# Optimization experiments

Measured on AMD Instinct MI355X. Metric: run time of the kernel, lower is better.

Reference implementation:

```python
import jax, jax.numpy as jnp
import numpy as np

EPS = 1e-5

def gn(x, w, b):
    # torch GroupNorm(num_groups=1, C) on [N, C]: normalize over channels per row
    m = jnp.mean(x, axis=-1, keepdims=True)
    v = jnp.mean((x - m) ** 2, axis=-1, keepdims=True)
    return (x - m) * jax.lax.rsqrt(v + EPS) * w + b

def att_layer(agts, ctr_d, hi, wi, nodes, p):
    (Wd1, bd1, Wd2, gnd2_w, gnd2_b, Wq, gnq_w, gnq_b,
     Wc1, gnc1_w, gnc1_b, Wc2, Wa, gnn_w, gnn_b, Wl, gnl_w, gnl_b) = p
    res = agts
    # dist MLP on edge ctr differences [E,2]
    d = jax.nn.relu(ctr_d @ Wd1.T + bd1)                     # [E, n_ctx]
    d = jax.nn.relu(gn(d @ Wd2.T, gnd2_w, gnd2_b))           # [E, n_ctx]
    # query from gathered actor features
    q = jax.nn.relu(gn(agts[hi] @ Wq.T, gnq_w, gnq_b))       # [E, n_ctx]
    # context: concat(dist, query, gathered lane feats) -> MLP
    cf = jnp.concatenate([d, q, nodes[wi]], axis=-1)         # [E, 3*n_ctx]
    cf = jax.nn.relu(gn(cf @ Wc1.T, gnc1_w, gnc1_b))         # [E, n_agt]
    cf = cf @ Wc2.T                                          # [E, n_agt]
    # scatter-aggregate onto actors
    a = agts @ Wa.T
    a = a.at[hi].add(cf)
    a = jax.nn.relu(gn(a, gnn_w, gnn_b))
    a = gn(a @ Wl.T, gnl_w, gnl_b)  # Linear with act=False
    return jax.nn.relu(a + res)

def setup_inputs() -> dict:
    key = jax.random.key(0)
    ks = jax.random.split(key, 20)
    M, N, E, D = 4000, 20000, 150000, 128
    s2 = 1.0 / np.sqrt(2.0)
    s128 = 1.0 / np.sqrt(128.0)
    s384 = 1.0 / np.sqrt(384.0)
    inp = {}
    inp["actors"] = jax.random.normal(ks[0], (M, D), jnp.float32)
    inp["nodes"] = jax.random.normal(ks[1], (N, D), jnp.float32)
    inp["actor_ctrs"] = jax.random.uniform(ks[2], (M, 2), jnp.float32)
    inp["node_ctrs"] = jax.random.uniform(ks[3], (N, 2), jnp.float32)
    inp["hi"] = jax.random.randint(ks[4], (E,), 0, M, dtype=jnp.int32)
    inp["wi"] = jax.random.randint(ks[5], (E,), 0, N, dtype=jnp.int32)
    inp["Wd1"] = jax.random.normal(ks[6], (2, D, 2), jnp.float32) * s2
    inp["bd1"] = jnp.zeros((2, D), jnp.float32)
    inp["Wd2"] = jax.random.normal(ks[7], (2, D, D), jnp.float32) * s128
    inp["gnd2_w"] = jnp.ones((2, D), jnp.float32)
    inp["gnd2_b"] = jnp.zeros((2, D), jnp.float32)
    inp["Wq"] = jax.random.normal(ks[8], (2, D, D), jnp.float32) * s128
    inp["gnq_w"] = jnp.ones((2, D), jnp.float32)
    inp["gnq_b"] = jnp.zeros((2, D), jnp.float32)
    inp["Wc1"] = jax.random.normal(ks[9], (2, D, 3 * D), jnp.float32) * s384
    inp["gnc1_w"] = jnp.ones((2, D), jnp.float32)
    inp["gnc1_b"] = jnp.zeros((2, D), jnp.float32)
    inp["Wc2"] = jax.random.normal(ks[10], (2, D, D), jnp.float32) * s128
    inp["Wa"] = jax.random.normal(ks[11], (2, D, D), jnp.float32) * s128
    inp["gnn_w"] = jnp.ones((2, D), jnp.float32)
    inp["gnn_b"] = jnp.zeros((2, D), jnp.float32)
    inp["Wl"] = jax.random.normal(ks[12], (2, D, D), jnp.float32) * s128
    inp["gnl_w"] = jnp.ones((2, D), jnp.float32)
    inp["gnl_b"] = jnp.zeros((2, D), jnp.float32)
    return inp

def reference(actors, nodes, actor_ctrs, node_ctrs, hi, wi,
              Wd1, bd1, Wd2, gnd2_w, gnd2_b, Wq, gnq_w, gnq_b,
              Wc1, gnc1_w, gnc1_b, Wc2, Wa, gnn_w, gnn_b, Wl, gnl_w, gnl_b):
    ctr_d = actor_ctrs[hi] - node_ctrs[wi]  # [E, 2], same edges for both layers
    stacked = (Wd1, bd1, Wd2, gnd2_w, gnd2_b, Wq, gnq_w, gnq_b,
               Wc1, gnc1_w, gnc1_b, Wc2, Wa, gnn_w, gnn_b, Wl, gnl_w, gnl_b)
    agts = actors
    for i in range(2):  # two Att layers
        p = tuple(t[i] for t in stacked)
        agts = att_layer(agts, ctr_d, hi, wi, nodes, p)
    return agts
```

## Files before the change

### kernel.cpp

```cpp
#include <hip/hip_runtime.h>

#define M_ACT 4000
#define NNODE 20000
#define NE 150000
#define DD 128
#define NT_E 586
#define NB_N2 313
#define ASTR 136
#define WSTR 72
#define BSTR 136

typedef __attribute__((ext_vector_type(8))) short bh8;
typedef __attribute__((ext_vector_type(4))) float vf4;

#define MFMA16(a, b, c) __builtin_amdgcn_mfma_f32_16x16x32_bf16((a), (b), (c), 0, 0, 0)
#define LGKM0() __asm__ volatile("s_waitcnt lgkmcnt(0)" ::: "memory")

__device__ __forceinline__ unsigned short f2bf(float f) {
    unsigned u = __float_as_uint(f);
    u = (u + 0x7fffu + ((u >> 16) & 1u)) >> 16;
    return (unsigned short)u;
}
__device__ __forceinline__ float bf2f(unsigned short s) {
    return __uint_as_float(((unsigned)s) << 16);
}

__device__ __forceinline__ void gn_stats8(const vf4* acc, float* mean, float* rs) {
    float s[4], q[4];
#pragma unroll
    for (int i = 0; i < 4; i++) {
        float a = 0.f, b = 0.f;
#pragma unroll
        for (int t = 0; t < 8; t++) { float v = acc[t][i]; a += v; b += v * v; }
        s[i] = a; q[i] = b;
    }
#pragma unroll
    for (int m = 1; m < 16; m <<= 1) {
#pragma unroll
        for (int i = 0; i < 4; i++) {
            s[i] += __shfl_xor(s[i], m, 64);
            q[i] += __shfl_xor(q[i], m, 64);
        }
    }
#pragma unroll
    for (int i = 0; i < 4; i++) {
        float mu = s[i] * (1.0f / 128.0f);
        float var = q[i] * (1.0f / 128.0f) - mu * mu;
        mean[i] = mu;
        rs[i] = rsqrtf(var + 1e-5f);
    }
}

template <bool RELU>
__device__ __forceinline__ void gn_to_lds(const vf4* acc, const float* __restrict__ gw,
                                          const float* __restrict__ gb, unsigned short* sm,
                                          int stride, int cb, int r0, int grp, int lm) {
    float mean[4], rs[4];
    gn_stats8(acc, mean, rs);
#pragma unroll
    for (int t = 0; t < 8; t++) {
        int c = 16 * t + lm;
        float w = gw[c], b = gb[c];
#pragma unroll
        for (int i = 0; i < 4; i++) {
            float y = (acc[t][i] - mean[i]) * rs[i] * w + b;
            if (RELU) y = fmaxf(y, 0.0f);
            sm[(r0 + grp * 4 + i) * stride + cb + c] = f2bf(y);
        }
    }
}

__device__ __forceinline__ void load_chunk(const unsigned short* __restrict__ src,
                                           unsigned short* dst, int tid) {
    for (int idx = tid; idx < 1152; idx += 256) {
        *(uint4*)&dst[idx * 8] = *(const uint4*)&src[idx * 8];
    }
}

__global__ __launch_bounds__(256, 2) void q2_kernel(const float* __restrict__ agts,
                                                    const unsigned short* __restrict__ wblob_l,
                                                    const float* __restrict__ gnq_w,
                                                    const float* __restrict__ gnq_b,
                                                    float* __restrict__ Q2) {
    __shared__ unsigned short smA[64 * ASTR];
    __shared__ unsigned short smW[128 * WSTR];
    const int tid = threadIdx.x;
    const int wave = tid >> 6, lane = tid & 63, grp = lane >> 4, lm = lane & 15;
    const int m0 = blockIdx.x * 64;
    const int r0 = wave * 16;
    const int arow = r0 + lm;

    for (int idx = tid; idx < 64 * 32; idx += 256) {
        int r = idx >> 5, q = idx & 31;
        int m = m0 + r;
        if (m >= M_ACT) m = 0;
        const float4 v = *(const float4*)(agts + (size_t)m * DD + q * 4);
        unsigned lo = (unsigned)f2bf(v.x) | ((unsigned)f2bf(v.y) << 16);
        unsigned hi2 = (unsigned)f2bf(v.z) | ((unsigned)f2bf(v.w) << 16);
        *(uint2*)&smA[r * ASTR + q * 4] = make_uint2(lo, hi2);
    }
    __syncthreads();

    vf4 acc[8];
#pragma unroll
    for (int t = 0; t < 8; t++) acc[t] = (vf4){0.f, 0.f, 0.f, 0.f};
    for (int ch = 0; ch < 2; ch++) {
        load_chunk(wblob_l + (2 + ch) * 9216, smW, tid);
        __syncthreads();
#pragma unroll
        for (int k0 = 0; k0 < 64; k0 += 32) {
            bh8 a = *(const bh8*)&smA[arow * ASTR + ch * 64 + k0 + grp * 8];
#pragma unroll
            for (int t = 0; t < 8; t++) {
                bh8 b = *(const bh8*)&smW[(16 * t + lm) * WSTR + k0 + grp * 8];
                acc[t] = MFMA16(a, b, acc[t]);
            }
        }
        __syncthreads();
    }
    gn_to_lds<true>(acc, gnq_w, gnq_b, smA, ASTR, 0, r0, grp, lm);

#pragma unroll
    for (int t = 0; t < 8; t++) acc[t] = (vf4){0.f, 0.f, 0.f, 0.f};
    for (int ch = 0; ch < 2; ch++) {
        load_chunk(wblob_l + (6 + ch) * 9216, smW, tid);
        __syncthreads();
#pragma unroll
        for (int k0 = 0; k0 < 64; k0 += 32) {
            bh8 a = *(const bh8*)&smA[arow * ASTR + ch * 64 + k0 + grp * 8];
#pragma unroll
            for (int t = 0; t < 8; t++) {
                bh8 b = *(const bh8*)&smW[(16 * t + lm) * WSTR + k0 + grp * 8];
                acc[t] = MFMA16(a, b, acc[t]);
            }
        }
        __syncthreads();
    }
#pragma unroll
    for (int t = 0; t < 8; t++) {
        int c = 16 * t + lm;
#pragma unroll
        for (int i = 0; i < 4; i++) {
            int m = m0 + r0 + grp * 4 + i;
            if (m < M_ACT) Q2[(size_t)m * DD + c] = acc[t][i];
        }
    }
}

__global__ __launch_bounds__(256, 2) void n2_kernel(const float* __restrict__ nodes,
                                                    const unsigned short* __restrict__ wblob,
                                                    float* __restrict__ N2_0,
                                                    float* __restrict__ N2_1) {
    __shared__ unsigned short smA[64 * ASTR];
    __shared__ unsigned short smW[128 * WSTR];
    const int half = blockIdx.x / NB_N2;
    const int bx = blockIdx.x - half * NB_N2;
    const unsigned short* wblob_l = wblob + (size_t)half * 16 * 9216;
    float* __restrict__ N2 = half ? N2_1 : N2_0;
    const int tid = threadIdx.x;
    const int wave = tid >> 6, lane = tid & 63, grp = lane >> 4, lm = lane & 15;
    const int n0 = bx * 64;
    const int r0 = wave * 16;
    const int arow = r0 + lm;

    for (int idx = tid; idx < 64 * 32; idx += 256) {
        int r = idx >> 5, q = idx & 31;
        int n = n0 + r;
        if (n >= NNODE) n = 0;
        const float4 v = *(const float4*)(nodes + (size_t)n * DD + q * 4);
        unsigned lo = (unsigned)f2bf(v.x) | ((unsigned)f2bf(v.y) << 16);
        unsigned hi2 = (unsigned)f2bf(v.z) | ((unsigned)f2bf(v.w) << 16);
        *(uint2*)&smA[r * ASTR + q * 4] = make_uint2(lo, hi2);
    }
    __syncthreads();

    vf4 acc[8];
#pragma unroll
    for (int t = 0; t < 8; t++) acc[t] = (vf4){0.f, 0.f, 0.f, 0.f};
    for (int ch = 0; ch < 2; ch++) {
        load_chunk(wblob_l + (8 + ch) * 9216, smW, tid);
        __syncthreads();
#pragma unroll
        for (int k0 = 0; k0 < 64; k0 += 32) {
            bh8 a = *(const bh8*)&smA[arow * ASTR + ch * 64 + k0 + grp * 8];
#pragma unroll
            for (int t = 0; t < 8; t++) {
                bh8 b = *(const bh8*)&smW[(16 * t + lm) * WSTR + k0 + grp * 8];
                acc[t] = MFMA16(a, b, acc[t]);
            }
        }
        __syncthreads();
    }
#pragma unroll
    for (int t = 0; t < 8; t++) {
        int c = 16 * t + lm;
#pragma unroll
        for (int i = 0; i < 4; i++) {
            int n = n0 + r0 + grp * 4 + i;
            if (n < NNODE) N2[(size_t)n * DD + c] = acc[t][i];
        }
    }
}

__global__ __launch_bounds__(512, 2) void edge_kernel(
    const float* __restrict__ actor_ctrs, const float* __restrict__ node_ctrs,
    const float* __restrict__ Wd1_l, const float* __restrict__ bd1_l,
    const float* __restrict__ Q2, const float* __restrict__ N2,
    const int* __restrict__ hi_s, const int* __restrict__ wi_s,
    const unsigned short* __restrict__ wblob_l,
    const float* __restrict__ gnd2_w, const float* __restrict__ gnd2_b,
    const float* __restrict__ gnc1_w, const float* __restrict__ gnc1_b,
    float* __restrict__ ssum, int* __restrict__ ctr) {
    __shared__ unsigned short smW[4 * 9216];
    __shared__ unsigned short smBuf[8][32 * BSTR];
    __shared__ float smWd1[3][128];
    __shared__ int smTile;
    {
        const int src0[4] = {0, 1, 4, 5};
#pragma unroll
        for (int s = 0; s < 4; s++)
            for (int idx = threadIdx.x; idx < 1152; idx += 512)
                *(uint4*)&smW[s * 9216 + idx * 8] =
                    *(const uint4*)&wblob_l[src0[s] * 9216 + idx * 8];
        for (int t = threadIdx.x; t < 128; t += 512) {
            smWd1[0][t] = Wd1_l[2 * t + 0];
            smWd1[1][t] = Wd1_l[2 * t + 1];
            smWd1[2][t] = bd1_l[t];
        }
    }
    const int wave = threadIdx.x >> 6, lane = threadIdx.x & 63;
    const int grp = lane >> 4, lm = lane & 15;
    unsigned short* buf = smBuf[wave];

    while (true) {
        __syncthreads();
        if (threadIdx.x == 0) smTile = atomicAdd(ctr, 1);
        __syncthreads();
        int tile = smTile;
        if (tile >= NT_E) break;
        int j0 = tile * 256 + wave * 32;
        if (j0 >= NE) continue;

        vf4 acc[2][8];
        int hg[2][4], wg[2][4];
        float cx[2], cy[2];
#pragma unroll
        for (int rt = 0; rt < 2; rt++) {
            int r = j0 + rt * 16 + lm;
            if (r > NE - 1) r = NE - 1;
            int hr = hi_s[r], wr = wi_s[r];
            cx[rt] = actor_ctrs[hr * 2 + 0] - node_ctrs[wr * 2 + 0];
            cy[rt] = actor_ctrs[hr * 2 + 1] - node_ctrs[wr * 2 + 1];
#pragma unroll
            for (int i = 0; i < 4; i++) {
                int j = j0 + rt * 16 + grp * 4 + i;
                if (j > NE - 1) j = NE - 1;
                hg[rt][i] = hi_s[j];
                wg[rt][i] = wi_s[j];
            }
        }
        bh8 a1[2][4];
#pragma unroll
        for (int ks = 0; ks < 4; ks++) {
            float wx[8], wy[8], wb[8];
#pragma unroll
            for (int e = 0; e < 8; e++) {
                int c = ks * 32 + grp * 8 + e;
                wx[e] = smWd1[0][c];
                wy[e] = smWd1[1][c];
                wb[e] = smWd1[2][c];
            }
#pragma unroll
            for (int rt = 0; rt < 2; rt++) {
                bh8 v;
#pragma unroll
                for (int e = 0; e < 8; e++) {
                    float x = fmaf(cy[rt], wy[e], fmaf(cx[rt], wx[e], wb[e]));
                    v[e] = (short)f2bf(fmaxf(x, 0.f));
                }
                a1[rt][ks] = v;
            }
        }
#pragma unroll
        for (int rt = 0; rt < 2; rt++)
#pragma unroll
            for (int t = 0; t < 8; t++) acc[rt][t] = (vf4){0.f, 0.f, 0.f, 0.f};
#pragma unroll
        for (int ks = 0; ks < 4; ks++) {
            bh8 B[8];
#pragma unroll
            for (int t = 0; t < 8; t++)
                B[t] = *(const bh8*)&smW[(ks >> 1) * 9216 + (16 * t + lm) * WSTR +
                                         (ks & 1) * 32 + grp * 8];
#pragma unroll
            for (int rt = 0; rt < 2; rt++)
#pragma unroll
                for (int t = 0; t < 8; t++) acc[rt][t] = MFMA16(a1[rt][ks], B[t], acc[rt][t]);
        }
        LGKM0();
#pragma unroll
        for (int rt = 0; rt < 2; rt++) {
            float mean[4], rs[4];
            gn_stats8(acc[rt], mean, rs);
#pragma unroll
            for (int t = 0; t < 8; t++) {
                int c = 16 * t + lm;
                float w = gnd2_w[c], b = gnd2_b[c];
#pragma unroll
                for (int i = 0; i < 4; i++) {
                    float y = (acc[rt][t][i] - mean[i]) * rs[i] * w + b;
                    buf[(rt * 16 + grp * 4 + i) * BSTR + c] = f2bf(fmaxf(y, 0.f));
                }
            }
        }
        LGKM0();
#pragma unroll
        for (int rt = 0; rt < 2; rt++)
#pragma unroll
            for (int t = 0; t < 8; t++) acc[rt][t] = (vf4){0.f, 0.f, 0.f, 0.f};
#pragma unroll
        for (int ks = 0; ks < 4; ks++) {
            bh8 B[8];
#pragma unroll
            for (int t = 0; t < 8; t++)
                B[t] = *(const bh8*)&smW[(2 + (ks >> 1)) * 9216 + (16 * t + lm) * WSTR +
                                         (ks & 1) * 32 + grp * 8];
#pragma unroll
            for (int rt = 0; rt < 2; rt++) {
                bh8 a = *(const bh8*)&buf[(rt * 16 + lm) * BSTR + ks * 32 + grp * 8];
#pragma unroll
                for (int t = 0; t < 8; t++) acc[rt][t] = MFMA16(a, B[t], acc[rt][t]);
            }
        }
#pragma unroll
        for (int rt = 0; rt < 2; rt++)
#pragma unroll
            for (int t = 0; t < 8; t++) {
                int c = 16 * t + lm;
#pragma unroll
                for (int i = 0; i < 4; i++)
                    acc[rt][t][i] +=
                        Q2[(size_t)hg[rt][i] * DD + c] + N2[(size_t)wg[rt][i] * DD + c];
            }
#pragma unroll
        for (int rt = 0; rt < 2; rt++) {
            float mean[4], rs[4];
            gn_stats8(acc[rt], mean, rs);
#pragma unroll
            for (int t = 0; t < 8; t++) {
                int c = 16 * t + lm;
                float w = gnc1_w[c], b = gnc1_b[c];
#pragma unroll
                for (int i = 0; i < 4; i++) {
                    float y = (acc[rt][t][i] - mean[i]) * rs[i] * w + b;
                    acc[rt][t][i] = fmaxf(y, 0.f);
                }
            }
        }
        {
            int hrem[2][4];
#pragma unroll
            for (int rt = 0; rt < 2; rt++)
#pragma unroll
                for (int i = 0; i < 4; i++) {
                    int j = j0 + rt * 16 + grp * 4 + i;
                    hrem[rt][i] = (j < NE) ? hg[rt][i] : -1;
                }
            while (true) {
                int hmin = 0x7fffffff;
#pragma unroll
                for (int rt = 0; rt < 2; rt++)
#pragma unroll
                    for (int i = 0; i < 4; i++)
                        if (hrem[rt][i] >= 0 && hrem[rt][i] < hmin) hmin = hrem[rt][i];
                hmin = min(hmin, __shfl_xor(hmin, 16, 64));
                hmin = min(hmin, __shfl_xor(hmin, 32, 64));
                if (hmin == 0x7fffffff) break;
                float p[8];
#pragma unroll
                for (int t = 0; t < 8; t++) p[t] = 0.f;
#pragma unroll
                for (int rt = 0; rt < 2; rt++)
#pragma unroll
                    for (int i = 0; i < 4; i++)
                        if (hrem[rt][i] == hmin) {
#pragma unroll
                            for (int t = 0; t < 8; t++) p[t] += acc[rt][t][i];
                            hrem[rt][i] = -1;
                        }
#pragma unroll
                for (int t = 0; t < 8; t++) {
                    p[t] += __shfl_xor(p[t], 16, 64);
                    p[t] += __shfl_xor(p[t], 32, 64);
                }
                if (grp == 0) {
#pragma unroll
                    for (int t = 0; t < 8; t++)
                        atomicAdd(&ssum[(size_t)hmin * DD + 16 * t + lm], p[t]);
                }
            }
        }
    }
}

__global__ __launch_bounds__(256, 2) void actor_kernel(
    const float* __restrict__ agts, const float* __restrict__ ssum,
    const float* __restrict__ gnn_w, const float* __restrict__ gnn_b,
    const float* __restrict__ gnl_w, const float* __restrict__ gnl_b,
    const unsigned short* __restrict__ wblob_l, float* __restrict__ dst) {
    __shared__ unsigned short smA[64 * ASTR];
    __shared__ unsigned short smW[128 * WSTR];
    const int tid = threadIdx.x;
    const int wave = tid >> 6, lane = tid & 63, grp = lane >> 4, lm = lane & 15;
    const int m0 = blockIdx.x * 64;
    const int r0 = wave * 16;
    const int arow = r0 + lm;

    for (int idx = tid; idx < 64 * 32; idx += 256) {
        int r = idx >> 5, q = idx & 31;
        int m = m0 + r;
        if (m >= M_ACT) m = 0;
        const float4 v = *(const float4*)(ssum + (size_t)m * DD + q * 4);
        unsigned lo = (unsigned)f2bf(v.x) | ((unsigned)f2bf(v.y) << 16);
        unsigned hi2 = (unsigned)f2bf(v.z) | ((unsigned)f2bf(v.w) << 16);
        *(uint2*)&smA[r * ASTR + q * 4] = make_uint2(lo, hi2);
    }
    __syncthreads();

    vf4 acc[8];
#pragma unroll
    for (int t = 0; t < 8; t++) acc[t] = (vf4){0.f, 0.f, 0.f, 0.f};
    for (int ch = 0; ch < 2; ch++) {
        load_chunk(wblob_l + (10 + ch) * 9216, smW, tid);
        __syncthreads();
#pragma unroll
        for (int k0 = 0; k0 < 64; k0 += 32) {
            bh8 a = *(const bh8*)&smA[arow * ASTR + ch * 64 + k0 + grp * 8];
#pragma unroll
            for (int t = 0; t < 8; t++) {
                bh8 b = *(const bh8*)&smW[(16 * t + lm) * WSTR + k0 + grp * 8];
                acc[t] = MFMA16(a, b, acc[t]);
            }
        }
        __syncthreads();
    }
    for (int idx = tid; idx < 64 * 32; idx += 256) {
        int r = idx >> 5, q = idx & 31;
        int m = m0 + r;
        if (m >= M_ACT) m = 0;
        const float4 v = *(const float4*)(agts + (size_t)m * DD + q * 4);
        unsigned lo = (unsigned)f2bf(v.x) | ((unsigned)f2bf(v.y) << 16);
        unsigned hi2 = (unsigned)f2bf(v.z) | ((unsigned)f2bf(v.w) << 16);
        *(uint2*)&smA[r * ASTR + q * 4] = make_uint2(lo, hi2);
    }
    __syncthreads();
    for (int ch = 0; ch < 2; ch++) {
        load_chunk(wblob_l + (12 + ch) * 9216, smW, tid);
        __syncthreads();
#pragma unroll
        for (int k0 = 0; k0 < 64; k0 += 32) {
            bh8 a = *(const bh8*)&smA[arow * ASTR + ch * 64 + k0 + grp * 8];
#pragma unroll
            for (int t = 0; t < 8; t++) {
                bh8 b = *(const bh8*)&smW[(16 * t + lm) * WSTR + k0 + grp * 8];
                acc[t] = MFMA16(a, b, acc[t]);
            }
        }
        __syncthreads();
    }
    gn_to_lds<true>(acc, gnn_w, gnn_b, smA, ASTR, 0, r0, grp, lm);

#pragma unroll
    for (int t = 0; t < 8; t++) acc[t] = (vf4){0.f, 0.f, 0.f, 0.f};
    for (int ch = 0; ch < 2; ch++) {
        load_chunk(wblob_l + (14 + ch) * 9216, smW, tid);
        __syncthreads();
#pragma unroll
        for (int k0 = 0; k0 < 64; k0 += 32) {
            bh8 a = *(const bh8*)&smA[arow * ASTR + ch * 64 + k0 + grp * 8];
#pragma unroll
            for (int t = 0; t < 8; t++) {
                bh8 b = *(const bh8*)&smW[(16 * t + lm) * WSTR + k0 + grp * 8];
                acc[t] = MFMA16(a, b, acc[t]);
            }
        }
        __syncthreads();
    }
    {
        float mean[4], rs[4];
        gn_stats8(acc, mean, rs);
#pragma unroll
        for (int t = 0; t < 8; t++) {
            int c = 16 * t + lm;
            float w = gnl_w[c], b = gnl_b[c];
#pragma unroll
            for (int i = 0; i < 4; i++) {
                int m = m0 + r0 + grp * 4 + i;
                if (m < M_ACT) {
                    float y = (acc[t][i] - mean[i]) * rs[i] * w + b;
                    y += agts[(size_t)m * DD + c];
                    dst[(size_t)m * DD + c] = fmaxf(y, 0.f);
                }
            }
        }
    }
}

__global__ void hist_kernel(const int* __restrict__ hi, int* __restrict__ hist) {
    int e = blockIdx.x * 256 + threadIdx.x;
    if (e < NE) atomicAdd(&hist[hi[e]], 1);
}

__global__ void scan_kernel(const int* __restrict__ hist, int* __restrict__ offs,
                            int* __restrict__ cursor) {
    __shared__ int part[256];
    int t = threadIdx.x;
    int base = t * 16;
    int s = 0;
    if (base < M_ACT)
        for (int i = 0; i < 16; i++) s += hist[base + i];
    part[t] = s;
    __syncthreads();
    for (int d = 1; d < 256; d <<= 1) {
        int u = (t >= d) ? part[t - d] : 0;
        __syncthreads();
        part[t] += u;
        __syncthreads();
    }
    int excl = part[t] - s;
    if (base < M_ACT) {
        int run = excl;
        for (int i = 0; i < 16; i++) {
            offs[base + i] = run;
            cursor[base + i] = run;
            run += hist[base + i];
        }
        if (base + 16 == M_ACT) offs[M_ACT] = run;
    }
}

__global__ void scatter_kernel(const int* __restrict__ hi, const int* __restrict__ wi,
                               int* __restrict__ cursor, int* __restrict__ hi_s,
                               int* __restrict__ wi_s) {
    int e = blockIdx.x * 256 + threadIdx.x;
    if (e < NE) {
        int h = hi[e];
        int p = atomicAdd(&cursor[h], 1);
        hi_s[p] = h;
        wi_s[p] = wi[e];
    }
}

__global__ void convert_kernel(const float* __restrict__ Wd2, const float* __restrict__ Wq,
                               const float* __restrict__ Wc1, const float* __restrict__ Wc2,
                               const float* __restrict__ Wa, const float* __restrict__ Wl,
                               unsigned short* __restrict__ wblob) {
    int ci = blockIdx.x;
    int l = ci >> 4, r = ci & 15;
    const float* src;
    int kc, K;
    if (r < 2)       { src = Wd2 + l * 16384; kc = r;      K = 128; }
    else if (r < 4)  { src = Wq  + l * 16384; kc = r - 2;  K = 128; }
    else if (r < 10) { src = Wc1 + l * 49152; kc = r - 4;  K = 384; }
    else if (r < 12) { src = Wc2 + l * 16384; kc = r - 10; K = 128; }
    else if (r < 14) { src = Wa  + l * 16384; kc = r - 12; K = 128; }
    else             { src = Wl  + l * 16384; kc = r - 14; K = 128; }
    unsigned short* dst = wblob + (size_t)ci * 9216;
    for (int idx = threadIdx.x; idx < 9216; idx += 256) {
        int n = idx / 72, kk = idx - n * 72;
        float v = (kk < 64) ? src[n * K + kc * 64 + kk] : 0.f;
        dst[idx] = f2bf(v);
    }
}

extern "C" void kernel_launch(void* const* d_in, const int* in_sizes, int n_in,
                              void* d_out, int out_size, void* d_ws, size_t ws_size,
                              hipStream_t stream) {
    const float* actors = (const float*)d_in[0];
    const float* nodes = (const float*)d_in[1];
    const float* actor_ctrs = (const float*)d_in[2];
    const float* node_ctrs = (const float*)d_in[3];
    const int* hi = (const int*)d_in[4];
    const int* wi = (const int*)d_in[5];
    const float* Wd1 = (const float*)d_in[6];
    const float* bd1 = (const float*)d_in[7];
    const float* Wd2 = (const float*)d_in[8];
    const float* gnd2_w = (const float*)d_in[9];
    const float* gnd2_b = (const float*)d_in[10];
    const float* Wq = (const float*)d_in[11];
    const float* gnq_w = (const float*)d_in[12];
    const float* gnq_b = (const float*)d_in[13];
    const float* Wc1 = (const float*)d_in[14];
    const float* gnc1_w = (const float*)d_in[15];
    const float* gnc1_b = (const float*)d_in[16];
    const float* Wc2 = (const float*)d_in[17];
    const float* Wa = (const float*)d_in[18];
    const float* gnn_w = (const float*)d_in[19];
    const float* gnn_b = (const float*)d_in[20];
    const float* Wl = (const float*)d_in[21];
    const float* gnl_w = (const float*)d_in[22];
    const float* gnl_b = (const float*)d_in[23];
    float* out = (float*)d_out;

    char* ws = (char*)d_ws;
    unsigned short* wblob = (unsigned short*)ws;  ws += 2 * 16 * 9216 * 2;
    float* Q2 = (float*)ws;                       ws += (size_t)M_ACT * DD * 4;
    float* N2_0 = (float*)ws;                     ws += (size_t)NNODE * DD * 4;
    float* N2_1 = (float*)ws;                     ws += (size_t)NNODE * DD * 4;
    float* ssum0 = (float*)ws;                    ws += (size_t)M_ACT * DD * 4;
    float* ssum1 = (float*)ws;                    ws += (size_t)M_ACT * DD * 4;
    float* A1 = (float*)ws;                       ws += (size_t)M_ACT * DD * 4;
    int* hist = (int*)ws;                         ws += M_ACT * 4;
    int* offs = (int*)ws;                         ws += (M_ACT + 4) * 4;
    int* cursor = (int*)ws;                       ws += M_ACT * 4;
    int* hi_s = (int*)ws;                         ws += NE * 4;
    int* wi_s = (int*)ws;                         ws += NE * 4;
    int* ctr4 = (int*)ws;                         ws += 16;

    hipMemsetAsync(hist, 0, M_ACT * 4, stream);
    hipMemsetAsync(ctr4, 0, 16, stream);
    hipMemsetAsync(ssum0, 0, (size_t)M_ACT * DD * 4 * 2, stream);
    hist_kernel<<<(NE + 255) / 256, 256, 0, stream>>>(hi, hist);
    scan_kernel<<<1, 256, 0, stream>>>(hist, offs, cursor);
    scatter_kernel<<<(NE + 255) / 256, 256, 0, stream>>>(hi, wi, cursor, hi_s, wi_s);
    convert_kernel<<<32, 256, 0, stream>>>(Wd2, Wq, Wc1, Wc2, Wa, Wl, wblob);

    const unsigned short* wb0 = wblob;
    const unsigned short* wb1 = wblob + 16 * 9216;
    const int AB = (M_ACT + 63) / 64;

    n2_kernel<<<2 * NB_N2, 256, 0, stream>>>(nodes, wblob, N2_0, N2_1);

    q2_kernel<<<AB, 256, 0, stream>>>(actors, wb0, gnq_w, gnq_b, Q2);
    edge_kernel<<<256, 512, 0, stream>>>(actor_ctrs, node_ctrs, Wd1, bd1, Q2, N2_0, hi_s,
                                         wi_s, wb0, gnd2_w, gnd2_b, gnc1_w, gnc1_b, ssum0,
                                         &ctr4[0]);
    actor_kernel<<<AB, 256, 0, stream>>>(actors, ssum0, gnn_w, gnn_b, gnl_w, gnl_b, wb0, A1);
    q2_kernel<<<AB, 256, 0, stream>>>(A1, wb1, gnq_w + 128, gnq_b + 128, Q2);
    edge_kernel<<<256, 512, 0, stream>>>(actor_ctrs, node_ctrs, Wd1 + 256, bd1 + 128, Q2,
                                         N2_1, hi_s, wi_s, wb1, gnd2_w + 128, gnd2_b + 128,
                                         gnc1_w + 128, gnc1_b + 128, ssum1, &ctr4[1]);
    actor_kernel<<<AB, 256, 0, stream>>>(A1, ssum1, gnn_w + 128, gnn_b + 128, gnl_w + 128,
                                         gnl_b + 128, wb1, out);
}
```

Measured before the change: 320.9 us.

## Merge setup, scatter, projection and actor kernels to cut launch count

The three memsets become one. The histogram and weight conversion run as one setup launch. The edge scatter, node projections and first-layer query projection run as one heterogeneous launch. The layer-0 actor update is fused with the layer-1 query projection so A1 is reused from LDS. This removes several kernel launches and serialization gaps plus a global round trip for A1. The cost is heterogeneous blocks whose work may be unbalanced, and more code per kernel.

```diff
diff --git a/kernel.cpp b/kernel.cpp
--- a/kernel.cpp
+++ b/kernel.cpp
@@ -6,6 +6,8 @@
 #define DD 128
 #define NT_E 586
 #define NB_N2 313
+#define HB 587
+#define AB 63
 #define ASTR 136
 #define WSTR 72
 #define BSTR 136
@@ -77,19 +79,186 @@
     }
 }
 
-__global__ __launch_bounds__(256, 2) void q2_kernel(const float* __restrict__ agts,
-                                                    const unsigned short* __restrict__ wblob_l,
-                                                    const float* __restrict__ gnq_w,
-                                                    const float* __restrict__ gnq_b,
-                                                    float* __restrict__ Q2) {
+__device__ __forceinline__ void q2_body(unsigned short* smA, unsigned short* smW,
+                                        const unsigned short* __restrict__ wq,
+                                        const unsigned short* __restrict__ wc,
+                                        const float* __restrict__ gnq_w,
+                                        const float* __restrict__ gnq_b,
+                                        float* __restrict__ Q2, int m0, int tid) {
+    const int wave = tid >> 6, lane = tid & 63, grp = lane >> 4, lm = lane & 15;
+    const int r0 = wave * 16;
+    const int arow = r0 + lm;
+    vf4 acc[8];
+#pragma unroll
+    for (int t = 0; t < 8; t++) acc[t] = (vf4){0.f, 0.f, 0.f, 0.f};
+    for (int ch = 0; ch < 2; ch++) {
+        load_chunk(wq + ch * 9216, smW, tid);
+        __syncthreads();
+#pragma unroll
+        for (int k0 = 0; k0 < 64; k0 += 32) {
+            bh8 a = *(const bh8*)&smA[arow * ASTR + ch * 64 + k0 + grp * 8];
+#pragma unroll
+            for (int t = 0; t < 8; t++) {
+                bh8 b = *(const bh8*)&smW[(16 * t + lm) * WSTR + k0 + grp * 8];
+                acc[t] = MFMA16(a, b, acc[t]);
+            }
+        }
+        __syncthreads();
+    }
+    gn_to_lds<true>(acc, gnq_w, gnq_b, smA, ASTR, 0, r0, grp, lm);
+
+#pragma unroll
+    for (int t = 0; t < 8; t++) acc[t] = (vf4){0.f, 0.f, 0.f, 0.f};
+    for (int ch = 0; ch < 2; ch++) {
+        load_chunk(wc + ch * 9216, smW, tid);
+        __syncthreads();
+#pragma unroll
+        for (int k0 = 0; k0 < 64; k0 += 32) {
+            bh8 a = *(const bh8*)&smA[arow * ASTR + ch * 64 + k0 + grp * 8];
+#pragma unroll
+            for (int t = 0; t < 8; t++) {
+                bh8 b = *(const bh8*)&smW[(16 * t + lm) * WSTR + k0 + grp * 8];
+                acc[t] = MFMA16(a, b, acc[t]);
+            }
+        }
+        __syncthreads();
+    }
+#pragma unroll
+    for (int t = 0; t < 8; t++) {
+        int c = 16 * t + lm;
+#pragma unroll
+        for (int i = 0; i < 4; i++) {
+            int m = m0 + r0 + grp * 4 + i;
+            if (m < M_ACT) Q2[(size_t)m * DD + c] = acc[t][i];
+        }
+    }
+}
+
+__global__ void setup_kernel(const int* __restrict__ hi, int* __restrict__ hist,
+                             const float* __restrict__ Wd2, const float* __restrict__ Wq,
+                             const float* __restrict__ Wc1, const float* __restrict__ Wc2,
+                             const float* __restrict__ Wa, const float* __restrict__ Wl,
+                             unsigned short* __restrict__ wblob) {
+    int b = blockIdx.x;
+    if (b < HB) {
+        int e = b * 256 + threadIdx.x;
+        if (e < NE) atomicAdd(&hist[hi[e]], 1);
+        return;
+    }
+    int ci = b - HB;
+    int l = ci >> 4, r = ci & 15;
+    const float* src;
+    int kc, K;
+    if (r < 2)       { src = Wd2 + l * 16384; kc = r;      K = 128; }
+    else if (r < 4)  { src = Wq  + l * 16384; kc = r - 2;  K = 128; }
+    else if (r < 10) { src = Wc1 + l * 49152; kc = r - 4;  K = 384; }
+    else if (r < 12) { src = Wc2 + l * 16384; kc = r - 10; K = 128; }
+    else if (r < 14) { src = Wa  + l * 16384; kc = r - 12; K = 128; }
+    else             { src = Wl  + l * 16384; kc = r - 14; K = 128; }
+    unsigned short* dst = wblob + (size_t)ci * 9216;
+    for (int idx = threadIdx.x; idx < 9216; idx += 256) {
+        int n = idx / 72, kk = idx - n * 72;
+        float v = (kk < 64) ? src[n * K + kc * 64 + kk] : 0.f;
+        dst[idx] = f2bf(v);
+    }
+}
+
+__global__ void scan_kernel(const int* __restrict__ hist, int* __restrict__ cursor) {
+    __shared__ int part[256];
+    int t = threadIdx.x;
+    int base = t * 16;
+    int s = 0;
+    if (base < M_ACT)
+        for (int i = 0; i < 16; i++) s += hist[base + i];
+    part[t] = s;
+    __syncthreads();
+    for (int d = 1; d < 256; d <<= 1) {
+        int u = (t >= d) ? part[t - d] : 0;
+        __syncthreads();
+        part[t] += u;
+        __syncthreads();
+    }
+    int excl = part[t] - s;
+    if (base < M_ACT) {
+        int run = excl;
+        for (int i = 0; i < 16; i++) {
+            cursor[base + i] = run;
+            run += hist[base + i];
+        }
+    }
+}
+
+__global__ __launch_bounds__(256, 2) void mega0_kernel(
+    const int* __restrict__ hi, const int* __restrict__ wi, int* __restrict__ cursor,
+    int* __restrict__ hi_s, int* __restrict__ wi_s, const float* __restrict__ nodes,
+    const unsigned short* __restrict__ wblob, float* __restrict__ N2_0,
+    float* __restrict__ N2_1, const float* __restrict__ agts,
+    const float* __restrict__ gnq_w, const float* __restrict__ gnq_b,
+    float* __restrict__ Q2) {
     __shared__ unsigned short smA[64 * ASTR];
     __shared__ unsigned short smW[128 * WSTR];
     const int tid = threadIdx.x;
+    int b = blockIdx.x;
+    if (b < HB) {
+        int e = b * 256 + tid;
+        if (e < NE) {
+            int h = hi[e];
+            int p = atomicAdd(&cursor[h], 1);
+            hi_s[p] = h;
+            wi_s[p] = wi[e];
+        }
+        return;
+    }
+    b -= HB;
     const int wave = tid >> 6, lane = tid & 63, grp = lane >> 4, lm = lane & 15;
-    const int m0 = blockIdx.x * 64;
     const int r0 = wave * 16;
     const int arow = r0 + lm;
-
+    if (b < 2 * NB_N2) {
+        const int half = b / NB_N2;
+        const int bx = b - half * NB_N2;
+        const unsigned short* wblob_l = wblob + (size_t)half * 16 * 9216;
+        float* __restrict__ N2 = half ? N2_1 : N2_0;
+        const int n0 = bx * 64;
+        for (int idx = tid; idx < 64 * 32; idx += 256) {
+            int r = idx >> 5, q = idx & 31;
+            int n = n0 + r;
+            if (n >= NNODE) n = 0;
+            const float4 v = *(const float4*)(nodes + (size_t)n * DD + q * 4);
+            unsigned lo = (unsigned)f2bf(v.x) | ((unsigned)f2bf(v.y) << 16);
+            unsigned hi2 = (unsigned)f2bf(v.z) | ((unsigned)f2bf(v.w) << 16);
+            *(uint2*)&smA[r * ASTR + q * 4] = make_uint2(lo, hi2);
+        }
+        __syncthreads();
+        vf4 acc[8];
+#pragma unroll
+        for (int t = 0; t < 8; t++) acc[t] = (vf4){0.f, 0.f, 0.f, 0.f};
+        for (int ch = 0; ch < 2; ch++) {
+            load_chunk(wblob_l + (8 + ch) * 9216, smW, tid);
+            __syncthreads();
+#pragma unroll
+            for (int k0 = 0; k0 < 64; k0 += 32) {
+                bh8 a = *(const bh8*)&smA[arow * ASTR + ch * 64 + k0 + grp * 8];
+#pragma unroll
+                for (int t = 0; t < 8; t++) {
+                    bh8 bb = *(const bh8*)&smW[(16 * t + lm) * WSTR + k0 + grp * 8];
+                    acc[t] = MFMA16(a, bb, acc[t]);
+                }
+            }
+            __syncthreads();
+        }
+#pragma unroll
+        for (int t = 0; t < 8; t++) {
+            int c = 16 * t + lm;
+#pragma unroll
+            for (int i = 0; i < 4; i++) {
+                int n = n0 + r0 + grp * 4 + i;
+                if (n < NNODE) N2[(size_t)n * DD + c] = acc[t][i];
+            }
+        }
+        return;
+    }
+    b -= 2 * NB_N2;
+    const int m0 = b * 64;
     for (int idx = tid; idx < 64 * 32; idx += 256) {
         int r = idx >> 5, q = idx & 31;
         int m = m0 + r;
@@ -100,106 +269,7 @@
         *(uint2*)&smA[r * ASTR + q * 4] = make_uint2(lo, hi2);
     }
     __syncthreads();
-
-    vf4 acc[8];
-#pragma unroll
-    for (int t = 0; t < 8; t++) acc[t] = (vf4){0.f, 0.f, 0.f, 0.f};
-    for (int ch = 0; ch < 2; ch++) {
-        load_chunk(wblob_l + (2 + ch) * 9216, smW, tid);
-        __syncthreads();
-#pragma unroll
-        for (int k0 = 0; k0 < 64; k0 += 32) {
-            bh8 a = *(const bh8*)&smA[arow * ASTR + ch * 64 + k0 + grp * 8];
-#pragma unroll
-            for (int t = 0; t < 8; t++) {
-                bh8 b = *(const bh8*)&smW[(16 * t + lm) * WSTR + k0 + grp * 8];
-                acc[t] = MFMA16(a, b, acc[t]);
-            }
-        }
-        __syncthreads();
-    }
-    gn_to_lds<true>(acc, gnq_w, gnq_b, smA, ASTR, 0, r0, grp, lm);
-
-#pragma unroll
-    for (int t = 0; t < 8; t++) acc[t] = (vf4){0.f, 0.f, 0.f, 0.f};
-    for (int ch = 0; ch < 2; ch++) {
-        load_chunk(wblob_l + (6 + ch) * 9216, smW, tid);
-        __syncthreads();
-#pragma unroll
-        for (int k0 = 0; k0 < 64; k0 += 32) {
-            bh8 a = *(const bh8*)&smA[arow * ASTR + ch * 64 + k0 + grp * 8];
-#pragma unroll
-            for (int t = 0; t < 8; t++) {
-                bh8 b = *(const bh8*)&smW[(16 * t + lm) * WSTR + k0 + grp * 8];
-                acc[t] = MFMA16(a, b, acc[t]);
-            }
-        }
-        __syncthreads();
-    }
-#pragma unroll
-    for (int t = 0; t < 8; t++) {
-        int c = 16 * t + lm;
-#pragma unroll
-        for (int i = 0; i < 4; i++) {
-            int m = m0 + r0 + grp * 4 + i;
-            if (m < M_ACT) Q2[(size_t)m * DD + c] = acc[t][i];
-        }
-    }
-}
-
-__global__ __launch_bounds__(256, 2) void n2_kernel(const float* __restrict__ nodes,
-                                                    const unsigned short* __restrict__ wblob,
-                                                    float* __restrict__ N2_0,
-                                                    float* __restrict__ N2_1) {
-    __shared__ unsigned short smA[64 * ASTR];
-    __shared__ unsigned short smW[128 * WSTR];
-    const int half = blockIdx.x / NB_N2;
-    const int bx = blockIdx.x - half * NB_N2;
-    const unsigned short* wblob_l = wblob + (size_t)half * 16 * 9216;
-    float* __restrict__ N2 = half ? N2_1 : N2_0;
-    const int tid = threadIdx.x;
-    const int wave = tid >> 6, lane = tid & 63, grp = lane >> 4, lm = lane & 15;
-    const int n0 = bx * 64;
-    const int r0 = wave * 16;
-    const int arow = r0 + lm;
-
-    for (int idx = tid; idx < 64 * 32; idx += 256) {
-        int r = idx >> 5, q = idx & 31;
-        int n = n0 + r;
-        if (n >= NNODE) n = 0;
-        const float4 v = *(const float4*)(nodes + (size_t)n * DD + q * 4);
-        unsigned lo = (unsigned)f2bf(v.x) | ((unsigned)f2bf(v.y) << 16);
-        unsigned hi2 = (unsigned)f2bf(v.z) | ((unsigned)f2bf(v.w) << 16);
-        *(uint2*)&smA[r * ASTR + q * 4] = make_uint2(lo, hi2);
-    }
-    __syncthreads();
-
-    vf4 acc[8];
-#pragma unroll
-    for (int t = 0; t < 8; t++) acc[t] = (vf4){0.f, 0.f, 0.f, 0.f};
-    for (int ch = 0; ch < 2; ch++) {
-        load_chunk(wblob_l + (8 + ch) * 9216, smW, tid);
-        __syncthreads();
-#pragma unroll
-        for (int k0 = 0; k0 < 64; k0 += 32) {
-            bh8 a = *(const bh8*)&smA[arow * ASTR + ch * 64 + k0 + grp * 8];
-#pragma unroll
-            for (int t = 0; t < 8; t++) {
-                bh8 b = *(const bh8*)&smW[(16 * t + lm) * WSTR + k0 + grp * 8];
-                acc[t] = MFMA16(a, b, acc[t]);
-            }
-        }
-        __syncthreads();
-    }
-#pragma unroll
-    for (int t = 0; t < 8; t++) {
-        int c = 16 * t + lm;
-#pragma unroll
-        for (int i = 0; i < 4; i++) {
-            int n = n0 + r0 + grp * 4 + i;
-            if (n < NNODE) N2[(size_t)n * DD + c] = acc[t][i];
-        }
-    }
+    q2_body(smA, smW, wblob + 2 * 9216, wblob + 6 * 9216, gnq_w, gnq_b, Q2, m0, tid);
 }
 
 __global__ __launch_bounds__(512, 2) void edge_kernel(
@@ -403,6 +473,115 @@
     }
 }
 
+__global__ __launch_bounds__(256, 2) void actor_q2_kernel(
+    const float* __restrict__ agts, const float* __restrict__ ssum,
+    const float* __restrict__ gnn_w, const float* __restrict__ gnn_b,
+    const float* __restrict__ gnl_w, const float* __restrict__ gnl_b,
+    const unsigned short* __restrict__ wblob, float* __restrict__ A1,
+    const float* __restrict__ gnq_w1, const float* __restrict__ gnq_b1,
+    float* __restrict__ Q2) {
+    __shared__ unsigned short smA[64 * ASTR];
+    __shared__ unsigned short smW[128 * WSTR];
+    const int tid = threadIdx.x;
+    const int wave = tid >> 6, lane = tid & 63, grp = lane >> 4, lm = lane & 15;
+    const int m0 = blockIdx.x * 64;
+    const int r0 = wave * 16;
+    const int arow = r0 + lm;
+
+    for (int idx = tid; idx < 64 * 32; idx += 256) {
+        int r = idx >> 5, q = idx & 31;
+        int m = m0 + r;
+        if (m >= M_ACT) m = 0;
+        const float4 v = *(const float4*)(ssum + (size_t)m * DD + q * 4);
+        unsigned lo = (unsigned)f2bf(v.x) | ((unsigned)f2bf(v.y) << 16);
+        unsigned hi2 = (unsigned)f2bf(v.z) | ((unsigned)f2bf(v.w) << 16);
+        *(uint2*)&smA[r * ASTR + q * 4] = make_uint2(lo, hi2);
+    }
+    __syncthreads();
+
+    vf4 acc[8];
+#pragma unroll
+    for (int t = 0; t < 8; t++) acc[t] = (vf4){0.f, 0.f, 0.f, 0.f};
+    for (int ch = 0; ch < 2; ch++) {
+        load_chunk(wblob + (10 + ch) * 9216, smW, tid);
+        __syncthreads();
+#pragma unroll
+        for (int k0 = 0; k0 < 64; k0 += 32) {
+            bh8 a = *(const bh8*)&smA[arow * ASTR + ch * 64 + k0 + grp * 8];
+#pragma unroll
+            for (int t = 0; t < 8; t++) {
+                bh8 b = *(const bh8*)&smW[(16 * t + lm) * WSTR + k0 + grp * 8];
+                acc[t] = MFMA16(a, b, acc[t]);
+            }
+        }
+        __syncthreads();
+    }
+    for (int idx = tid; idx < 64 * 32; idx += 256) {
+        int r = idx >> 5, q = idx & 31;
+        int m = m0 + r;
+        if (m >= M_ACT) m = 0;
+        const float4 v = *(const float4*)(agts + (size_t)m * DD + q * 4);
+        unsigned lo = (unsigned)f2bf(v.x) | ((unsigned)f2bf(v.y) << 16);
+        unsigned hi2 = (unsigned)f2bf(v.z) | ((unsigned)f2bf(v.w) << 16);
+        *(uint2*)&smA[r * ASTR + q * 4] = make_uint2(lo, hi2);
+    }
+    __syncthreads();
+    for (int ch = 0; ch < 2; ch++) {
+        load_chunk(wblob + (12 + ch) * 9216, smW, tid);
+        __syncthreads();
+#pragma unroll
+        for (int k0 = 0; k0 < 64; k0 += 32) {
+            bh8 a = *(const bh8*)&smA[arow * ASTR + ch * 64 + k0 + grp * 8];
+#pragma unroll
+            for (int t = 0; t < 8; t++) {
+                bh8 b = *(const bh8*)&smW[(16 * t + lm) * WSTR + k0 + grp * 8];
+                acc[t] = MFMA16(a, b, acc[t]);
+            }
+        }
+        __syncthreads();
+    }
+    gn_to_lds<true>(acc, gnn_w, gnn_b, smA, ASTR, 0, r0, grp, lm);
+
+#pragma unroll
+    for (int t = 0; t < 8; t++) acc[t] = (vf4){0.f, 0.f, 0.f, 0.f};
+    for (int ch = 0; ch < 2; ch++) {
+        load_chunk(wblob + (14 + ch) * 9216, smW, tid);
+        __syncthreads();
+#pragma unroll
+        for (int k0 = 0; k0 < 64; k0 += 32) {
+            bh8 a = *(const bh8*)&smA[arow * ASTR + ch * 64 + k0 + grp * 8];
+#pragma unroll
+            for (int t = 0; t < 8; t++) {
+                bh8 b = *(const bh8*)&smW[(16 * t + lm) * WSTR + k0 + grp * 8];
+                acc[t] = MFMA16(a, b, acc[t]);
+            }
+        }
+        __syncthreads();
+    }
+    {
+        float mean[4], rs[4];
+        gn_stats8(acc, mean, rs);
+#pragma unroll
+        for (int t = 0; t < 8; t++) {
+            int c = 16 * t + lm;
+            float w = gnl_w[c], b = gnl_b[c];
+#pragma unroll
+            for (int i = 0; i < 4; i++) {
+                int m = m0 + r0 + grp * 4 + i;
+                float y = (acc[t][i] - mean[i]) * rs[i] * w + b;
+                float o = 0.f;
+                if (m < M_ACT) {
+                    o = fmaxf(y + agts[(size_t)m * DD + c], 0.f);
+                    A1[(size_t)m * DD + c] = o;
+                }
+                smA[(r0 + grp * 4 + i) * ASTR + c] = f2bf(o);
+            }
+        }
+    }
+    q2_body(smA, smW, wblob + (16 + 2) * 9216, wblob + (16 + 6) * 9216, gnq_w1, gnq_b1, Q2,
+            m0, tid);
+}
+
 __global__ __launch_bounds__(256, 2) void actor_kernel(
     const float* __restrict__ agts, const float* __restrict__ ssum,
     const float* __restrict__ gnn_w, const float* __restrict__ gnn_b,
@@ -503,73 +682,6 @@
                 }
             }
         }
-    }
-}
-
-__global__ void hist_kernel(const int* __restrict__ hi, int* __restrict__ hist) {
-    int e = blockIdx.x * 256 + threadIdx.x;
-    if (e < NE) atomicAdd(&hist[hi[e]], 1);
-}
-
-__global__ void scan_kernel(const int* __restrict__ hist, int* __restrict__ offs,
-                            int* __restrict__ cursor) {
-    __shared__ int part[256];
-    int t = threadIdx.x;
-    int base = t * 16;
-    int s = 0;
-    if (base < M_ACT)
-        for (int i = 0; i < 16; i++) s += hist[base + i];
-    part[t] = s;
-    __syncthreads();
-    for (int d = 1; d < 256; d <<= 1) {
-        int u = (t >= d) ? part[t - d] : 0;
-        __syncthreads();
-        part[t] += u;
-        __syncthreads();
-    }
-    int excl = part[t] - s;
-    if (base < M_ACT) {
-        int run = excl;
-        for (int i = 0; i < 16; i++) {
-            offs[base + i] = run;
-            cursor[base + i] = run;
-            run += hist[base + i];
-        }
-        if (base + 16 == M_ACT) offs[M_ACT] = run;
-    }
-}
-
-__global__ void scatter_kernel(const int* __restrict__ hi, const int* __restrict__ wi,
-                               int* __restrict__ cursor, int* __restrict__ hi_s,
-                               int* __restrict__ wi_s) {
-    int e = blockIdx.x * 256 + threadIdx.x;
-    if (e < NE) {
-        int h = hi[e];
-        int p = atomicAdd(&cursor[h], 1);
-        hi_s[p] = h;
-        wi_s[p] = wi[e];
-    }
-}
-
-__global__ void convert_kernel(const float* __restrict__ Wd2, const float* __restrict__ Wq,
-                               const float* __restrict__ Wc1, const float* __restrict__ Wc2,
-                               const float* __restrict__ Wa, const float* __restrict__ Wl,
-                               unsigned short* __restrict__ wblob) {
-    int ci = blockIdx.x;
-    int l = ci >> 4, r = ci & 15;
-    const float* src;
-    int kc, K;
-    if (r < 2)       { src = Wd2 + l * 16384; kc = r;      K = 128; }
-    else if (r < 4)  { src = Wq  + l * 16384; kc = r - 2;  K = 128; }
-    else if (r < 10) { src = Wc1 + l * 49152; kc = r - 4;  K = 384; }
-    else if (r < 12) { src = Wc2 + l * 16384; kc = r - 10; K = 128; }
-    else if (r < 14) { src = Wa  + l * 16384; kc = r - 12; K = 128; }
-    else             { src = Wl  + l * 16384; kc = r - 14; K = 128; }
-    unsigned short* dst = wblob + (size_t)ci * 9216;
-    for (int idx = threadIdx.x; idx < 9216; idx += 256) {
-        int n = idx / 72, kk = idx - n * 72;
-        float v = (kk < 64) ? src[n * K + kc * 64 + kk] : 0.f;
-        dst[idx] = f2bf(v);
     }
 }
 
@@ -607,36 +719,32 @@
     float* Q2 = (float*)ws;                       ws += (size_t)M_ACT * DD * 4;
     float* N2_0 = (float*)ws;                     ws += (size_t)NNODE * DD * 4;
     float* N2_1 = (float*)ws;                     ws += (size_t)NNODE * DD * 4;
-    float* ssum0 = (float*)ws;                    ws += (size_t)M_ACT * DD * 4;
-    float* ssum1 = (float*)ws;                    ws += (size_t)M_ACT * DD * 4;
     float* A1 = (float*)ws;                       ws += (size_t)M_ACT * DD * 4;
-    int* hist = (int*)ws;                         ws += M_ACT * 4;
-    int* offs = (int*)ws;                         ws += (M_ACT + 4) * 4;
     int* cursor = (int*)ws;                       ws += M_ACT * 4;
     int* hi_s = (int*)ws;                         ws += NE * 4;
     int* wi_s = (int*)ws;                         ws += NE * 4;
-    int* ctr4 = (int*)ws;                         ws += 16;
-
-    hipMemsetAsync(hist, 0, M_ACT * 4, stream);
-    hipMemsetAsync(ctr4, 0, 16, stream);
-    hipMemsetAsync(ssum0, 0, (size_t)M_ACT * DD * 4 * 2, stream);
-    hist_kernel<<<(NE + 255) / 256, 256, 0, stream>>>(hi, hist);
-    scan_kernel<<<1, 256, 0, stream>>>(hist, offs, cursor);
-    scatter_kernel<<<(NE + 255) / 256, 256, 0, stream>>>(hi, wi, cursor, hi_s, wi_s);
-    convert_kernel<<<32, 256, 0, stream>>>(Wd2, Wq, Wc1, Wc2, Wa, Wl, wblob);
+    char* zbase = ws;
+    int* hist = (int*)ws;                         ws += M_ACT * 4;
+    int* ctr4 = (int*)ws;                         ws += 64;
+    float* ssum0 = (float*)ws;                    ws += (size_t)M_ACT * DD * 4;
+    float* ssum1 = (float*)ws;                    ws += (size_t)M_ACT * DD * 4;
+    const size_t zbytes = (size_t)(ws - zbase);
+
+    hipMemsetAsync(zbase, 0, zbytes, stream);
+    setup_kernel<<<HB + 32, 256, 0, stream>>>(hi, hist, Wd2, Wq, Wc1, Wc2, Wa, Wl, wblob);
+    scan_kernel<<<1, 256, 0, stream>>>(hist, cursor);
 
     const unsigned short* wb0 = wblob;
     const unsigned short* wb1 = wblob + 16 * 9216;
-    const int AB = (M_ACT + 63) / 64;
-
-    n2_kernel<<<2 * NB_N2, 256, 0, stream>>>(nodes, wblob, N2_0, N2_1);
-
-    q2_kernel<<<AB, 256, 0, stream>>>(actors, wb0, gnq_w, gnq_b, Q2);
+
+    mega0_kernel<<<HB + 2 * NB_N2 + AB, 256, 0, stream>>>(hi, wi, cursor, hi_s, wi_s, nodes,
+                                                          wblob, N2_0, N2_1, actors, gnq_w,
+                                                          gnq_b, Q2);
     edge_kernel<<<256, 512, 0, stream>>>(actor_ctrs, node_ctrs, Wd1, bd1, Q2, N2_0, hi_s,
                                          wi_s, wb0, gnd2_w, gnd2_b, gnc1_w, gnc1_b, ssum0,
                                          &ctr4[0]);
-    actor_kernel<<<AB, 256, 0, stream>>>(actors, ssum0, gnn_w, gnn_b, gnl_w, gnl_b, wb0, A1);
-    q2_kernel<<<AB, 256, 0, stream>>>(A1, wb1, gnq_w + 128, gnq_b + 128, Q2);
+    actor_q2_kernel<<<AB, 256, 0, stream>>>(actors, ssum0, gnn_w, gnn_b, gnl_w, gnl_b, wblob,
+                                            A1, gnq_w + 128, gnq_b + 128, Q2);
     edge_kernel<<<256, 512, 0, stream>>>(actor_ctrs, node_ctrs, Wd1 + 256, bd1 + 128, Q2,
                                          N2_1, hi_s, wi_s, wb1, gnd2_w + 128, gnd2_b + 128,
                                          gnc1_w + 128, gnc1_b + 128, ssum1, &ctr4[1]);
```

Result: faster. 299.6 us (-6.7%).
